# Performance work log

Hardware: AMD Instinct MI355X
Metric: run time of the kernel (lower is better)

The kernel has to match this reference:

```python
import jax, jax.numpy as jnp
import numpy as np

N = 50000      # nodes
E = 800000     # edges
F_IN = 256
HID = [256, 256, 512]
G = 512        # graphs
FP = 2048      # fingerprint size


def setup_inputs() -> dict:
    key = jax.random.key(0)
    ks = jax.random.split(key, 14)
    node_features = jax.random.normal(ks[0], (N, F_IN), dtype=jnp.float32)
    edge_index = jax.random.randint(ks[1], (2, E), 0, N, dtype=jnp.int64)
    batch = jnp.sort(jax.random.randint(ks[2], (N,), 0, G, dtype=jnp.int64))

    def lin(k, fi, fo):
        s = 1.0 / np.sqrt(fi)
        kw, kb = jax.random.split(k)
        W = jax.random.uniform(kw, (fi, fo), jnp.float32, -s, s)
        b = jax.random.uniform(kb, (fo,), jnp.float32, -s, s)
        return W, b

    W1, b1 = lin(ks[3], F_IN, HID[0])
    W2, b2 = lin(ks[4], HID[0], HID[1])
    W3, b3 = lin(ks[5], HID[1], HID[2])
    pw, pb = lin(ks[6], HID[2], 1)          # PoolWeightedSum gating linear
    Wo, bo = lin(ks[7], 2 * HID[2], FP)     # head: weight_sum + max concat
    return dict(node_features=node_features, edge_index=edge_index, batch=batch,
                W1=W1, b1=b1, W2=W2, b2=b2, W3=W3, b3=b3,
                pw=pw, pb=pb, Wo=Wo, bo=bo)


def _gcn_layer(x, src, dst, W, b):
    # GCNConv: add self-loops, symmetric normalization, h = x @ W, aggregate.
    n = x.shape[0]
    h = x @ W  # [N, F_out]
    loop = jnp.arange(n, dtype=src.dtype)
    s = jnp.concatenate([src, loop])
    d = jnp.concatenate([dst, loop])
    deg = jax.ops.segment_sum(jnp.ones(s.shape[0], h.dtype), d, num_segments=n)
    dis = jax.lax.rsqrt(deg)  # deg >= 1 because of self-loops
    norm = dis[s] * dis[d]    # [E+N]
    out = jax.ops.segment_sum(h[s] * norm[:, None], d, num_segments=n)
    return out + b


def _forward(node_features, edge_index, batch,
             W1, b1, W2, b2, W3, b3, pw, pb, Wo, bo):
    src, dst = edge_index[0], edge_index[1]
    x = node_features
    for W, b in ((W1, b1), (W2, b2), (W3, b3)):
        x = jax.nn.relu(_gcn_layer(x, src, dst, W, b))

    # PoolWeightedSum: sigmoid-gated node features, scatter-add per graph
    w = jax.nn.sigmoid(x @ pw + pb)  # [N, 1]
    pooled_ws = jax.ops.segment_sum(x * w, batch, num_segments=G,
                                    indices_are_sorted=True)
    # PoolMax: scatter-max per graph (empty segments -> 0, like torch zeros init)
    pooled_max = jax.ops.segment_max(x, batch, num_segments=G,
                                     indices_are_sorted=True)
    pooled_max = jnp.where(jnp.isfinite(pooled_max), pooled_max, 0.0)

    feats = jnp.concatenate([pooled_ws, pooled_max], axis=1)  # [G, 2*HID[-1]]
    return jax.nn.relu(feats @ Wo + bo)  # [G, FP]


def reference(node_features, edge_index, batch,
              W1, b1, W2, b2, W3, b3, pw, pb, Wo, bo):
    return _forward(node_features, edge_index, batch,
                    W1, b1, W2, b2, W3, b3, pw, pb, Wo, bo)
```

## Files before the change

kernel.cpp:

```cpp
#include <hip/hip_runtime.h>
#include <math.h>

#define NNODES 50000
#define NEDGES 800000
#define NGRAPH 512
#define FIN    256
#define H1     256
#define H2     256
#define H3     512
#define FPOUT  2048

#define NBUCK  196
#define EPB    3200
#define BCAP   4864

typedef __attribute__((ext_vector_type(8))) short short8;
typedef __attribute__((ext_vector_type(8))) _Float16 half8;
typedef __attribute__((ext_vector_type(4))) float floatx4;
typedef __attribute__((ext_vector_type(4))) unsigned short ushx4;

__device__ inline float h2f(ushort u) { return (float)__builtin_bit_cast(_Float16, u); }
__device__ inline ushort f2h(float x) { return __builtin_bit_cast(ushort, (_Float16)x); }
__device__ inline void split2h(float a, ushort& h, ushort& l) {
    _Float16 hh = (_Float16)a;
    h = __builtin_bit_cast(ushort, hh);
    l = f2h(a - (float)hh);
}


__global__ __launch_bounds__(256) void zero_i32(int* p, int n) {
    int i = blockIdx.x * 256 + threadIdx.x;
    if (i < n) p[i] = 0;
}

__global__ __launch_bounds__(256) void count_deg(const int* __restrict__ ei, int* __restrict__ degi, int e_total) {
    int e = blockIdx.x * 256 + threadIdx.x;
    if (e >= e_total) return;
    int d = ei[e_total + e];
    atomicAdd(&degi[d], 1);
}

__global__ __launch_bounds__(256) void calc_dis(const int* __restrict__ degi, float* __restrict__ dis, int n) {
    int i = blockIdx.x * 256 + threadIdx.x;
    if (i < n) dis[i] = rsqrtf((float)(degi[i] + 1));
}

__global__ __launch_bounds__(256) void scanA(const int* __restrict__ degi, int* __restrict__ offs,
                                             int* __restrict__ partials, int n) {
    __shared__ int sm[256];
    int t = threadIdx.x, idx = blockIdx.x * 256 + t;
    int v = (idx < n) ? degi[idx] : 0;
    sm[t] = v; __syncthreads();
    for (int d = 1; d < 256; d <<= 1) {
        int add = (t >= d) ? sm[t - d] : 0;
        __syncthreads();
        sm[t] += add;
        __syncthreads();
    }
    if (idx < n) offs[idx + 1] = sm[t];
    if (t == 255) partials[blockIdx.x] = sm[255];
}

__global__ __launch_bounds__(256) void scanB(int* __restrict__ partials, int nb) {
    __shared__ int sm[256];
    int t = threadIdx.x;
    int v = (t < nb) ? partials[t] : 0;
    sm[t] = v; __syncthreads();
    for (int d = 1; d < 256; d <<= 1) {
        int add = (t >= d) ? sm[t - d] : 0;
        __syncthreads();
        sm[t] += add;
        __syncthreads();
    }
    if (t < nb) partials[t] = sm[t] - v;
}

__global__ __launch_bounds__(256) void scanC(int* __restrict__ offs, const int* __restrict__ partials, int n) {
    int idx = blockIdx.x * 256 + threadIdx.x;
    if (idx < n) offs[idx + 1] += partials[blockIdx.x];
    if (idx == 0) offs[0] = 0;
}

__global__ __launch_bounds__(256) void binA(const int* __restrict__ ei, const int* __restrict__ offs,
                                            int* __restrict__ gcur, int2* __restrict__ tmp, int e_total) {
    __shared__ int2 ls[EPB];
    __shared__ int2 ls2[EPB];
    __shared__ int hist[256], lpref[256], lcur[256], gbase[256], obase[256];
    int tid = threadIdx.x;
    int e0 = blockIdx.x * EPB;
    int cnt = e_total - e0; if (cnt > EPB) cnt = EPB;
    hist[tid] = 0;
    __syncthreads();
    for (int i = tid; i < cnt; i += 256) {
        int s = ei[e0 + i];
        int d = ei[e_total + e0 + i];
        ls[i] = (int2){s, d};
        atomicAdd(&hist[d >> 8], 1);
    }
    __syncthreads();
    int hv = hist[tid];
    lpref[tid] = hv;
    __syncthreads();
    for (int dlt = 1; dlt < 256; dlt <<= 1) {
        int add = (tid >= dlt) ? lpref[tid - dlt] : 0;
        __syncthreads();
        lpref[tid] += add;
        __syncthreads();
    }
    int excl = lpref[tid] - hv;
    __syncthreads();
    lpref[tid] = excl;
    lcur[tid] = 0;
    __syncthreads();
    for (int i = tid; i < cnt; i += 256) {
        int2 pr = ls[i];
        int b = pr.y >> 8;
        int r = atomicAdd(&lcur[b], 1);
        ls2[lpref[b] + r] = pr;
    }
    if (tid < NBUCK) {
        int c = hist[tid];
        gbase[tid] = c ? atomicAdd(&gcur[tid], c) : 0;
        obase[tid] = offs[tid << 8];
    }
    __syncthreads();
    for (int i = tid; i < cnt; i += 256) {
        int2 pr = ls2[i];
        int b = pr.y >> 8;
        tmp[obase[b] + gbase[b] + (i - lpref[b])] = pr;
    }
}

__global__ __launch_bounds__(256) void binB(const int2* __restrict__ tmp, const int* __restrict__ offs,
                                            const float* __restrict__ dis, int2* __restrict__ csr_pair) {
    __shared__ int2 ls[BCAP];
    __shared__ int cntN[256];
    int tid = threadIdx.x;
    int b = blockIdx.x;
    int nlo = b << 8;
    int nhi = nlo + 256; if (nhi > NNODES) nhi = NNODES;
    int base = offs[nlo];
    int tot = offs[nhi] - base;
    cntN[tid] = 0;
    __syncthreads();
    for (int c0 = 0; c0 < tot; c0 += BCAP) {
        int cc = tot - c0; if (cc > BCAP) cc = BCAP;
        for (int i = tid; i < cc; i += 256)
            ls[i] = tmp[base + c0 + i];
        __syncthreads();
        for (int i = tid; i < cc; i += 256) {
            int2 pr = ls[i];
            int d = pr.y;
            int r = atomicAdd(&cntN[d & 255], 1);
            float w = dis[pr.x] * dis[d];
            csr_pair[offs[d] + r] = (int2){pr.x, __float_as_int(w)};
        }
        __syncthreads();
    }
}

__global__ __launch_bounds__(256) void wsplit_t(const float* __restrict__ W, ushort* __restrict__ hi,
                                                ushort* __restrict__ lo, int K, int N) {
    __shared__ float sm[32][33];
    int tx = threadIdx.x & 31, ty = threadIdx.x >> 5;
    int n0 = blockIdx.x * 32, k0 = blockIdx.y * 32;
    #pragma unroll
    for (int j = 0; j < 32; j += 8)
        sm[ty + j][tx] = W[(size_t)(k0 + ty + j) * N + n0 + tx];
    __syncthreads();
    #pragma unroll
    for (int j = 0; j < 32; j += 8) {
        float a = sm[tx][ty + j];
        ushort h, l; split2h(a, h, l);
        size_t o = (size_t)(n0 + ty + j) * K + k0 + tx;
        hi[o] = h; lo[o] = l;
    }
}

__global__ __launch_bounds__(256) void conv_f16(const float* __restrict__ x, ushort* __restrict__ xh, int total4) {
    int i = blockIdx.x * 256 + threadIdx.x;
    if (i >= total4) return;
    float4 a = ((const float4*)x)[i];
    ushx4 h = {f2h(a.x), f2h(a.y), f2h(a.z), f2h(a.w)};
    ((ushx4*)xh)[i] = h;
}

template<int SPLIT, int ACC, int KSPAN>
__global__ __launch_bounds__(256) void gemm_f16(const ushort* __restrict__ Ahp, const ushort* __restrict__ Alp,
                                                const ushort* __restrict__ Bhp, const ushort* __restrict__ Blp,
                                                float* __restrict__ C, ushort* __restrict__ Ch,
                                                const float* __restrict__ bias,
                                                int M, int N, int K, int do_relu, int outmode) {
    __shared__ _Float16 lsA[128 * 64];
    __shared__ _Float16 lsB[128 * 64];
    __shared__ _Float16 lsAl[SPLIT ? 128 * 64 : 8];
    __shared__ _Float16 lsBl[SPLIT ? 128 * 64 : 8];
    const _Float16* Ah = (const _Float16*)Ahp;
    const _Float16* Al = (const _Float16*)Alp;
    const _Float16* Bh = (const _Float16*)Bhp;
    const _Float16* Bl = (const _Float16*)Blp;

    int tid = threadIdx.x;
    int w = tid >> 6, lane = tid & 63;
    int quad = lane >> 4, lr = lane & 15;
    int wm = w & 1, wn = w >> 1;

    int gx = gridDim.x;
    int orig = blockIdx.y * gx + blockIdx.x;
    int nwg = gx * gridDim.y;
    int xcd = orig & 7, slot = orig >> 3;
    int q = nwg >> 3, r = nwg & 7;
    int wid = (xcd < r ? xcd * (q + 1) : r * (q + 1) + (xcd - r) * q) + slot;
    int row0 = (wid / gx) * 128, col0 = (wid % gx) * 128;
    int kb = blockIdx.z * KSPAN;

    floatx4 acc[4][4];
    #pragma unroll
    for (int i = 0; i < 4; ++i)
        #pragma unroll
        for (int j = 0; j < 4; ++j)
            acc[i][j] = (floatx4){0.f, 0.f, 0.f, 0.f};

    const half8 zer = {};
    int srow = tid >> 3;
    int sgran = tid & 7;
    int skk = sgran * 8;
    int sgx = (sgran ^ (srow & 7)) * 8;

    half8 pa[4], pb[4], pal[4], pbl[4];
    #pragma unroll
    for (int c = 0; c < 4; ++c) {
        int row = c * 32 + srow;
        bool mok = (row0 + row) < M;
        size_t aoff = (size_t)(row0 + row) * K + kb + skk;
        pa[c] = mok ? *(const half8*)(Ah + aoff) : zer;
        if constexpr (SPLIT) pal[c] = mok ? *(const half8*)(Al + aoff) : zer;
        size_t boff = (size_t)(col0 + row) * K + kb + skk;
        pb[c] = *(const half8*)(Bh + boff);
        if constexpr (SPLIT) pbl[c] = *(const half8*)(Bl + boff);
    }

    for (int k0 = kb; k0 < kb + KSPAN; k0 += 64) {
        #pragma unroll
        for (int c = 0; c < 4; ++c) {
            int lo = (c * 32 + srow) * 64 + sgx;
            *(half8*)(lsA + lo) = pa[c];
            *(half8*)(lsB + lo) = pb[c];
            if constexpr (SPLIT) { *(half8*)(lsAl + lo) = pal[c]; *(half8*)(lsBl + lo) = pbl[c]; }
        }
        __syncthreads();
        if (k0 + 64 < kb + KSPAN) {
            #pragma unroll
            for (int c = 0; c < 4; ++c) {
                int row = c * 32 + srow;
                bool mok = (row0 + row) < M;
                size_t aoff = (size_t)(row0 + row) * K + k0 + 64 + skk;
                pa[c] = mok ? *(const half8*)(Ah + aoff) : zer;
                if constexpr (SPLIT) pal[c] = mok ? *(const half8*)(Al + aoff) : zer;
                size_t boff = (size_t)(col0 + row) * K + k0 + 64 + skk;
                pb[c] = *(const half8*)(Bh + boff);
                if constexpr (SPLIT) pbl[c] = *(const half8*)(Bl + boff);
            }
        }
        #pragma unroll
        for (int kk = 0; kk < 2; ++kk) {
            half8 af[4], afl[4];
            #pragma unroll
            for (int mt = 0; mt < 4; ++mt) {
                int row = wm * 64 + mt * 16 + lr;
                int ao = row * 64 + (((kk * 4 + quad) ^ (row & 7)) << 3);
                af[mt] = *(const half8*)(lsA + ao);
                if constexpr (SPLIT) afl[mt] = *(const half8*)(lsAl + ao);
            }
            #pragma unroll
            for (int nt = 0; nt < 4; ++nt) {
                int row = wn * 64 + nt * 16 + lr;
                int bo = row * 64 + (((kk * 4 + quad) ^ (row & 7)) << 3);
                half8 bf = *(const half8*)(lsB + bo);
                half8 bfl;
                if constexpr (SPLIT) bfl = *(const half8*)(lsBl + bo);
                #pragma unroll
                for (int mt = 0; mt < 4; ++mt) {
                    acc[mt][nt] = __builtin_amdgcn_mfma_f32_16x16x32_f16(af[mt], bf, acc[mt][nt], 0, 0, 0);
                    if constexpr (SPLIT) {
                        acc[mt][nt] = __builtin_amdgcn_mfma_f32_16x16x32_f16(af[mt], bfl, acc[mt][nt], 0, 0, 0);
                        acc[mt][nt] = __builtin_amdgcn_mfma_f32_16x16x32_f16(afl[mt], bf, acc[mt][nt], 0, 0, 0);
                    }
                }
            }
        }
        __syncthreads();
    }

    size_t zoff = ACC ? (size_t)blockIdx.z * M * N : 0;
    #pragma unroll
    for (int mt = 0; mt < 4; ++mt) {
        #pragma unroll
        for (int rr = 0; rr < 4; ++rr) {
            int row = row0 + wm * 64 + mt * 16 + quad * 4 + rr;
            if (row >= M) continue;
            #pragma unroll
            for (int nt = 0; nt < 4; ++nt) {
                int col = col0 + wn * 64 + nt * 16 + lr;
                float v = acc[mt][nt][rr];
                if (!ACC) {
                    v += bias[col];
                    if (do_relu) v = v > 0.f ? v : 0.f;
                }
                if (outmode) Ch[(size_t)row * N + col] = f2h(v);
                else         C[zoff + (size_t)row * N + col] = v;
            }
        }
    }
}

__global__ __launch_bounds__(256) void head_fin(const float* __restrict__ part, const float* __restrict__ bo,
                                                float* __restrict__ out) {
    int i4 = blockIdx.x * 256 + threadIdx.x;
    const int TOT4 = NGRAPH * FPOUT / 4;
    if (i4 >= TOT4) return;
    int col4 = i4 & (FPOUT / 4 - 1);
    const size_t STRIDE4 = (size_t)NGRAPH * FPOUT / 4;
    const float4* p = (const float4*)part;
    float4 a = p[i4];
    float4 b = p[i4 + STRIDE4];
    float4 c = p[i4 + 2 * STRIDE4];
    float4 d = p[i4 + 3 * STRIDE4];
    float4 bb = ((const float4*)bo)[col4];
    float4 o;
    o.x = a.x + b.x + c.x + d.x + bb.x; o.x = o.x > 0.f ? o.x : 0.f;
    o.y = a.y + b.y + c.y + d.y + bb.y; o.y = o.y > 0.f ? o.y : 0.f;
    o.z = a.z + b.z + c.z + d.z + bb.z; o.z = o.z > 0.f ? o.z : 0.f;
    o.w = a.w + b.w + c.w + d.w + bb.w; o.w = o.w > 0.f ? o.w : 0.f;
    ((float4*)out)[i4] = o;
}

__global__ __launch_bounds__(256) void agg256b(const ushort* __restrict__ xh, ushort* __restrict__ yh,
                                               const float* __restrict__ dis,
                                               const int* __restrict__ offs, const int2* __restrict__ csr_pair) {
    constexpr int F = 256;
    int wave = threadIdx.x >> 6;
    int lane = threadIdx.x & 63;
    int half = lane >> 5;
    int sub  = lane & 31;
    int v = blockIdx.x * 8 + wave * 2 + half;
    int beg = offs[v], end = offs[v + 1];
    int len = end - beg;
    int leno = __shfl_xor(len, 32, 64);
    int maxlen = len > leno ? len : leno;

    float dv = dis[v];
    float sw = dv * dv;
    short8 a0 = ((const short8*)(xh + (size_t)v * F))[sub];
    float acc[8];
    #pragma unroll
    for (int j = 0; j < 8; ++j) acc[j] = h2f((ushort)a0[j]) * sw;

    for (int k = 0; k < maxlen; k += 8) {
        int   s[8];
        float w[8];
        #pragma unroll
        for (int u = 0; u < 8; ++u) {
            int idx = beg + k + u;
            bool val = idx < end;
            int ic = val ? idx : beg;
            int2 pr = csr_pair[ic];
            s[u] = pr.x;
            w[u] = val ? __int_as_float(pr.y) : 0.f;
        }
        short8 g[8];
        #pragma unroll
        for (int u = 0; u < 8; ++u)
            g[u] = ((const short8*)(xh + (size_t)s[u] * F))[sub];
        #pragma unroll
        for (int u = 0; u < 8; ++u) {
            #pragma unroll
            for (int j = 0; j < 8; ++j)
                acc[j] += h2f((ushort)g[u][j]) * w[u];
        }
    }

    ushort h[8];
    #pragma unroll
    for (int j = 0; j < 8; ++j) h[j] = f2h(acc[j]);
    short8 hv = {(short)h[0], (short)h[1], (short)h[2], (short)h[3], (short)h[4], (short)h[5], (short)h[6], (short)h[7]};
    ((short8*)(yh + (size_t)v * F))[sub] = hv;
}

__global__ __launch_bounds__(1024) void gatepool(const float* __restrict__ x, const float* __restrict__ pw,
                                                 const float* __restrict__ pb, const int* __restrict__ batch,
                                                 ushort* __restrict__ phi, ushort* __restrict__ plo, int n) {
    int g = blockIdx.x;
    int t = threadIdx.x;
    int wave = t >> 6, lane = t & 63;
    int lo_ = 0, hi_ = n;
    while (lo_ < hi_) { int mid = (lo_ + hi_) >> 1; if (batch[mid] < g) lo_ = mid + 1; else hi_ = mid; }
    int start = lo_;
    hi_ = n;
    while (lo_ < hi_) { int mid = (lo_ + hi_) >> 1; if (batch[mid] < g + 1) lo_ = mid + 1; else hi_ = mid; }
    int end = lo_;

    const float4* pwv = (const float4*)pw;
    float4 wa = pwv[lane], wb = pwv[lane + 64];
    float pb0 = pb[0];

    float4 s0 = make_float4(0.f, 0.f, 0.f, 0.f), s1 = s0;
    float4 m0 = make_float4(-INFINITY, -INFINITY, -INFINITY, -INFINITY), m1 = m0;

    for (int nn = start + wave; nn < end; nn += 16) {
        const float4* xr = (const float4*)(x + (size_t)nn * 512);
        float4 a = xr[lane];
        float4 b = xr[lane + 64];
        float p = a.x * wa.x + a.y * wa.y + a.z * wa.z + a.w * wa.w
                + b.x * wb.x + b.y * wb.y + b.z * wb.z + b.w * wb.w;
        #pragma unroll
        for (int off = 32; off; off >>= 1) p += __shfl_down(p, off, 64);
        float wg = __shfl(p, 0, 64);
        wg = 1.f / (1.f + expf(-(wg + pb0)));
        s0.x += a.x * wg; s0.y += a.y * wg; s0.z += a.z * wg; s0.w += a.w * wg;
        s1.x += b.x * wg; s1.y += b.y * wg; s1.z += b.z * wg; s1.w += b.w * wg;
        m0.x = fmaxf(m0.x, a.x); m0.y = fmaxf(m0.y, a.y); m0.z = fmaxf(m0.z, a.z); m0.w = fmaxf(m0.w, a.w);
        m1.x = fmaxf(m1.x, b.x); m1.y = fmaxf(m1.y, b.y); m1.z = fmaxf(m1.z, b.z); m1.w = fmaxf(m1.w, b.w);
    }

    __shared__ float ls[16][1024];
    *(float4*)&ls[wave][lane * 4]       = s0;
    *(float4*)&ls[wave][256 + lane * 4] = s1;
    *(float4*)&ls[wave][512 + lane * 4] = m0;
    *(float4*)&ls[wave][768 + lane * 4] = m1;
    __syncthreads();

    float val;
    if (t < 512) {
        float s = 0.f;
        #pragma unroll
        for (int wv = 0; wv < 16; ++wv) s += ls[wv][t];
        val = s;
    } else {
        float m = -INFINITY;
        #pragma unroll
        for (int wv = 0; wv < 16; ++wv) m = fmaxf(m, ls[wv][t]);
        if (start >= end) m = 0.f;
        val = m;
    }
    ushort h, l;
    split2h(val, h, l);
    size_t base = (size_t)g * 1024;
    phi[base + t] = h;
    plo[base + t] = l;
}


extern "C" void kernel_launch(void* const* d_in, const int* in_sizes, int n_in,
                              void* d_out, int out_size, void* d_ws, size_t ws_size,
                              hipStream_t stream) {
    const float* x0    = (const float*)d_in[0];
    const int*   ei    = (const int*)d_in[1];
    const int*   batch = (const int*)d_in[2];
    const float* W1 = (const float*)d_in[3];
    const float* b1 = (const float*)d_in[4];
    const float* W2 = (const float*)d_in[5];
    const float* b2 = (const float*)d_in[6];
    const float* W3 = (const float*)d_in[7];
    const float* b3 = (const float*)d_in[8];
    const float* pw = (const float*)d_in[9];
    const float* pb = (const float*)d_in[10];
    const float* Wo = (const float*)d_in[11];
    const float* bo = (const float*)d_in[12];
    float* out = (float*)d_out;

    float* ws = (float*)d_ws;
    size_t off = 0;
    float* bufB = ws + off; off += (size_t)NNODES * 512;
    ushort* xh  = (ushort*)(ws + off); off += (size_t)NNODES * 256 / 2;
    ushort* yh  = (ushort*)(ws + off); off += (size_t)NNODES * 256 / 2;
    int2*   tmp = (int2*)(ws + off);   off += (size_t)NNODES * 256 / 2;
    ushort* W1thi = (ushort*)(ws + off); off += 256 * 256 / 2;
    ushort* W1tlo = (ushort*)(ws + off); off += 256 * 256 / 2;
    ushort* W2thi = (ushort*)(ws + off); off += 256 * 256 / 2;
    ushort* W2tlo = (ushort*)(ws + off); off += 256 * 256 / 2;
    ushort* W3thi = (ushort*)(ws + off); off += 512 * 256 / 2;
    ushort* W3tlo = (ushort*)(ws + off); off += 512 * 256 / 2;
    ushort* Wothi = (ushort*)(ws + off); off += (size_t)FPOUT * 1024 / 2;
    ushort* Wotlo = (ushort*)(ws + off); off += (size_t)FPOUT * 1024 / 2;
    ushort* phi = (ushort*)(ws + off); off += (size_t)NGRAPH * 1024 / 2;
    ushort* plo = (ushort*)(ws + off); off += (size_t)NGRAPH * 1024 / 2;
    float* dis  = ws + off; off += NNODES;
    int*   degi = (int*)(ws + off); off += NNODES;
    int*   offs = (int*)(ws + off); off += (NNODES + 4);
    int*   gcur = (int*)(ws + off); off += 256;
    int2*  csr_pair = (int2*)(ws + off); off += 2 * (size_t)NEDGES;
    int*   partials = (int*)(ws + off); off += 256;

    const int NB_N = (NNODES + 255) / 256;
    const int NB_E = (NEDGES + 255) / 256;
    const int NB_A = NNODES / 8;
    const int MB128 = (NNODES + 127) / 128;

    { dim3 g(256 / 32, 256 / 32);    wsplit_t<<<g, 256, 0, stream>>>(W1, W1thi, W1tlo, 256, 256); }
    { dim3 g(256 / 32, 256 / 32);    wsplit_t<<<g, 256, 0, stream>>>(W2, W2thi, W2tlo, 256, 256); }
    { dim3 g(512 / 32, 256 / 32);    wsplit_t<<<g, 256, 0, stream>>>(W3, W3thi, W3tlo, 256, 512); }
    { dim3 g(FPOUT / 32, 1024 / 32); wsplit_t<<<g, 256, 0, stream>>>(Wo, Wothi, Wotlo, 1024, FPOUT); }

    zero_i32<<<NB_N, 256, 0, stream>>>(degi, NNODES);
    count_deg<<<NB_E, 256, 0, stream>>>(ei, degi, NEDGES);
    calc_dis<<<NB_N, 256, 0, stream>>>(degi, dis, NNODES);
    scanA<<<NB_N, 256, 0, stream>>>(degi, offs, partials, NNODES);
    scanB<<<1, 256, 0, stream>>>(partials, NB_N);
    scanC<<<NB_N, 256, 0, stream>>>(offs, partials, NNODES);
    zero_i32<<<1, 256, 0, stream>>>(gcur, 256);
    binA<<<NEDGES / EPB, 256, 0, stream>>>(ei, offs, gcur, tmp, NEDGES);
    binB<<<NBUCK, 256, 0, stream>>>(tmp, offs, dis, csr_pair);

    conv_f16<<<(NNODES * 256 / 4 + 255) / 256, 256, 0, stream>>>(x0, xh, NNODES * 256 / 4);

    agg256b<<<NB_A, 256, 0, stream>>>(xh, yh, dis, offs, csr_pair);
    {
        dim3 grid(H1 / 128, MB128);
        gemm_f16<0, 0, 256><<<grid, 256, 0, stream>>>(yh, nullptr, W1thi, nullptr, nullptr, xh, b1,
                                                      NNODES, H1, FIN, 1, 1);
    }
    agg256b<<<NB_A, 256, 0, stream>>>(xh, yh, dis, offs, csr_pair);
    {
        dim3 grid(H2 / 128, MB128);
        gemm_f16<0, 0, 256><<<grid, 256, 0, stream>>>(yh, nullptr, W2thi, nullptr, nullptr, xh, b2,
                                                      NNODES, H2, H1, 1, 1);
    }
    agg256b<<<NB_A, 256, 0, stream>>>(xh, yh, dis, offs, csr_pair);
    {
        dim3 grid(H3 / 128, MB128);
        gemm_f16<0, 0, 256><<<grid, 256, 0, stream>>>(yh, nullptr, W3thi, nullptr, bufB, nullptr, b3,
                                                      NNODES, H3, H2, 1, 0);
    }
    gatepool<<<NGRAPH, 1024, 0, stream>>>(bufB, pw, pb, batch, phi, plo, NNODES);
    {
        dim3 grid(FPOUT / 128, (NGRAPH + 127) / 128, 4);
        gemm_f16<1, 1, 256><<<grid, 256, 0, stream>>>(phi, plo, Wothi, Wotlo, bufB, nullptr, nullptr,
                                                      NGRAPH, FPOUT, 1024, 0, 0);
    }
    head_fin<<<(NGRAPH * FPOUT / 4 + 255) / 256, 256, 0, stream>>>(bufB, bo, out);
}
```

Measured before the change: 539.1 us.

## Aggregate in feature-chunked layout over degree-sorted nodes for gather locality

Stores the fp16 node features in a chunked layout of 32 features per chunk, [chunk][node][32], written by conv_f16 and by the GEMM epilogue. Nodes are reordered by degree through a histogram, scan and scatter into an aux table, so that nodes of similar degree share a wave. The new aggregation kernel handles one feature chunk per block and splits edges across 4 waves, then reduces through shared memory. The aim is to shrink the gathered working set per chunk so it fits in cache and to cut divergence from uneven degrees, at the cost of extra preprocessing kernels, a shared-memory reduction and eight times as many blocks.

```diff
diff --git a/kernel.cpp b/kernel.cpp
--- a/kernel.cpp
+++ b/kernel.cpp
@@ -159,6 +159,40 @@
     }
 }
 
+__global__ __launch_bounds__(256) void deg_hist(const int* __restrict__ degi, int* __restrict__ hist, int n) {
+    int i = blockIdx.x * 256 + threadIdx.x;
+    if (i >= n) return;
+    int d = degi[i];
+    atomicAdd(&hist[d > 255 ? 255 : d], 1);
+}
+
+__global__ __launch_bounds__(256) void scan256(int* __restrict__ buf) {
+    __shared__ int sm[256];
+    int t = threadIdx.x;
+    int v = buf[t];
+    sm[t] = v; __syncthreads();
+    for (int d = 1; d < 256; d <<= 1) {
+        int add = (t >= d) ? sm[t - d] : 0;
+        __syncthreads();
+        sm[t] += add;
+        __syncthreads();
+    }
+    buf[t] = sm[t] - v;
+}
+
+__global__ __launch_bounds__(256) void deg_scatter(const int* __restrict__ degi, const int* __restrict__ offs,
+                                                   const float* __restrict__ dis, const int* __restrict__ hbase,
+                                                   int* __restrict__ hcur, int4* __restrict__ aux, int n) {
+    int i = blockIdx.x * 256 + threadIdx.x;
+    if (i >= n) return;
+    int d = degi[i];
+    int b = d > 255 ? 255 : d;
+    int r = atomicAdd(&hcur[b], 1);
+    int4 e;
+    e.x = i; e.y = offs[i]; e.z = d; e.w = __float_as_int(dis[i]);
+    aux[hbase[b] + r] = e;
+}
+
 __global__ __launch_bounds__(256) void wsplit_t(const float* __restrict__ W, ushort* __restrict__ hi,
                                                 ushort* __restrict__ lo, int K, int N) {
     __shared__ float sm[32][33];
@@ -180,9 +214,12 @@
 __global__ __launch_bounds__(256) void conv_f16(const float* __restrict__ x, ushort* __restrict__ xh, int total4) {
     int i = blockIdx.x * 256 + threadIdx.x;
     if (i >= total4) return;
+    int n  = i >> 6;
+    int f4 = i & 63;
     float4 a = ((const float4*)x)[i];
     ushx4 h = {f2h(a.x), f2h(a.y), f2h(a.z), f2h(a.w)};
-    ((ushx4*)xh)[i] = h;
+    size_t o4 = (((size_t)(f4 >> 3) * NNODES + n) * 32 + (f4 & 7) * 4) >> 2;
+    ((ushx4*)xh)[o4] = h;
 }
 
 template<int SPLIT, int ACC, int KSPAN>
@@ -307,7 +344,7 @@
                     v += bias[col];
                     if (do_relu) v = v > 0.f ? v : 0.f;
                 }
-                if (outmode) Ch[(size_t)row * N + col] = f2h(v);
+                if (outmode) Ch[((size_t)(col >> 5) * M + row) * 32 + (col & 31)] = f2h(v);
                 else         C[zoff + (size_t)row * N + col] = v;
             }
         }
@@ -335,56 +372,70 @@
     ((float4*)out)[i4] = o;
 }
 
-__global__ __launch_bounds__(256) void agg256b(const ushort* __restrict__ xh, ushort* __restrict__ yh,
-                                               const float* __restrict__ dis,
-                                               const int* __restrict__ offs, const int2* __restrict__ csr_pair) {
-    constexpr int F = 256;
+__global__ __launch_bounds__(256) void agg_chunk(const ushort* __restrict__ xh, ushort* __restrict__ yh,
+                                                 const int4* __restrict__ aux,
+                                                 const int2* __restrict__ csr_pair) {
+    __shared__ float sm[4][64][9];
     int wave = threadIdx.x >> 6;
     int lane = threadIdx.x & 63;
-    int half = lane >> 5;
-    int sub  = lane & 31;
-    int v = blockIdx.x * 8 + wave * 2 + half;
-    int beg = offs[v], end = offs[v + 1];
-    int len = end - beg;
-    int leno = __shfl_xor(len, 32, 64);
-    int maxlen = len > leno ? len : leno;
-
-    float dv = dis[v];
+    int nd = lane >> 2, quad = lane & 3;
+    int chunk = blockIdx.x & 7;
+    int slot = (blockIdx.x >> 3) * 16 + nd;
+    int4 a = aux[slot];
+    int v = a.x, beg = a.y, deg = a.z;
+    float dv = __int_as_float(a.w);
     float sw = dv * dv;
-    short8 a0 = ((const short8*)(xh + (size_t)v * F))[sub];
+    const _Float16* xc = (const _Float16*)xh + (size_t)chunk * NNODES * 32;
+
     float acc[8];
+    if (wave == 0) {
+        half8 g0 = *(const half8*)(xc + (size_t)v * 32 + quad * 8);
+        #pragma unroll
+        for (int j = 0; j < 8; ++j) acc[j] = (float)g0[j] * sw;
+    } else {
+        #pragma unroll
+        for (int j = 0; j < 8; ++j) acc[j] = 0.f;
+    }
+
+    int md = deg;
     #pragma unroll
-    for (int j = 0; j < 8; ++j) acc[j] = h2f((ushort)a0[j]) * sw;
-
-    for (int k = 0; k < maxlen; k += 8) {
-        int   s[8];
-        float w[8];
-        #pragma unroll
-        for (int u = 0; u < 8; ++u) {
-            int idx = beg + k + u;
-            bool val = idx < end;
-            int ic = val ? idx : beg;
-            int2 pr = csr_pair[ic];
-            s[u] = pr.x;
+    for (int m = 4; m <= 32; m <<= 1) { int o = __shfl_xor(md, m, 64); md = md > o ? md : o; }
+
+    for (int k8 = 0; k8 < md; k8 += 8) {
+        int s[2]; float w[2];
+        #pragma unroll
+        for (int u = 0; u < 2; ++u) {
+            int e = k8 + u * 4 + wave;
+            bool val = e < deg;
+            int2 pr = csr_pair[val ? (beg + e) : beg];
+            s[u] = val ? pr.x : 0;
             w[u] = val ? __int_as_float(pr.y) : 0.f;
         }
-        short8 g[8];
-        #pragma unroll
-        for (int u = 0; u < 8; ++u)
-            g[u] = ((const short8*)(xh + (size_t)s[u] * F))[sub];
-        #pragma unroll
-        for (int u = 0; u < 8; ++u) {
+        half8 g[2];
+        #pragma unroll
+        for (int u = 0; u < 2; ++u)
+            g[u] = *(const half8*)(xc + (size_t)s[u] * 32 + quad * 8);
+        #pragma unroll
+        for (int u = 0; u < 2; ++u)
             #pragma unroll
-            for (int j = 0; j < 8; ++j)
-                acc[j] += h2f((ushort)g[u][j]) * w[u];
-        }
-    }
-
-    ushort h[8];
+            for (int j = 0; j < 8; ++j) acc[j] += (float)g[u][j] * w[u];
+    }
+
     #pragma unroll
-    for (int j = 0; j < 8; ++j) h[j] = f2h(acc[j]);
-    short8 hv = {(short)h[0], (short)h[1], (short)h[2], (short)h[3], (short)h[4], (short)h[5], (short)h[6], (short)h[7]};
-    ((short8*)(yh + (size_t)v * F))[sub] = hv;
+    for (int j = 0; j < 8; ++j) sm[wave][lane][j] = acc[j];
+    __syncthreads();
+    if (wave == 0) {
+        #pragma unroll
+        for (int wv = 1; wv < 4; ++wv)
+            #pragma unroll
+            for (int j = 0; j < 8; ++j) acc[j] += sm[wv][lane][j];
+        ushort h[8];
+        #pragma unroll
+        for (int j = 0; j < 8; ++j) h[j] = f2h(acc[j]);
+        short8 hv = {(short)h[0], (short)h[1], (short)h[2], (short)h[3],
+                     (short)h[4], (short)h[5], (short)h[6], (short)h[7]};
+        *(short8*)(yh + (size_t)v * 256 + chunk * 32 + quad * 8) = hv;
+    }
 }
 
 __global__ __launch_bounds__(1024) void gatepool(const float* __restrict__ x, const float* __restrict__ pw,
@@ -491,10 +542,13 @@
     int*   gcur = (int*)(ws + off); off += 256;
     int2*  csr_pair = (int2*)(ws + off); off += 2 * (size_t)NEDGES;
     int*   partials = (int*)(ws + off); off += 256;
+    int*   hist = (int*)(ws + off); off += 256;
+    int*   hcur = (int*)(ws + off); off += 256;
+    int4*  aux  = (int4*)(ws + off); off += (size_t)NNODES * 4;
 
     const int NB_N = (NNODES + 255) / 256;
     const int NB_E = (NEDGES + 255) / 256;
-    const int NB_A = NNODES / 8;
+    const int NB_A = (NNODES / 16) * 8;
     const int MB128 = (NNODES + 127) / 128;
 
     { dim3 g(256 / 32, 256 / 32);    wsplit_t<<<g, 256, 0, stream>>>(W1, W1thi, W1tlo, 256, 256); }
@@ -512,21 +566,27 @@
     binA<<<NEDGES / EPB, 256, 0, stream>>>(ei, offs, gcur, tmp, NEDGES);
     binB<<<NBUCK, 256, 0, stream>>>(tmp, offs, dis, csr_pair);
 
+    zero_i32<<<1, 256, 0, stream>>>(hist, 256);
+    deg_hist<<<NB_N, 256, 0, stream>>>(degi, hist, NNODES);
+    scan256<<<1, 256, 0, stream>>>(hist);
+    zero_i32<<<1, 256, 0, stream>>>(hcur, 256);
+    deg_scatter<<<NB_N, 256, 0, stream>>>(degi, offs, dis, hist, hcur, aux, NNODES);
+
     conv_f16<<<(NNODES * 256 / 4 + 255) / 256, 256, 0, stream>>>(x0, xh, NNODES * 256 / 4);
 
-    agg256b<<<NB_A, 256, 0, stream>>>(xh, yh, dis, offs, csr_pair);
+    agg_chunk<<<NB_A, 256, 0, stream>>>(xh, yh, aux, csr_pair);
     {
         dim3 grid(H1 / 128, MB128);
         gemm_f16<0, 0, 256><<<grid, 256, 0, stream>>>(yh, nullptr, W1thi, nullptr, nullptr, xh, b1,
                                                       NNODES, H1, FIN, 1, 1);
     }
-    agg256b<<<NB_A, 256, 0, stream>>>(xh, yh, dis, offs, csr_pair);
+    agg_chunk<<<NB_A, 256, 0, stream>>>(xh, yh, aux, csr_pair);
     {
         dim3 grid(H2 / 128, MB128);
         gemm_f16<0, 0, 256><<<grid, 256, 0, stream>>>(yh, nullptr, W2thi, nullptr, nullptr, xh, b2,
                                                       NNODES, H2, H1, 1, 1);
     }
-    agg256b<<<NB_A, 256, 0, stream>>>(xh, yh, dis, offs, csr_pair);
+    agg_chunk<<<NB_A, 256, 0, stream>>>(xh, yh, aux, csr_pair);
     {
         dim3 grid(H3 / 128, MB128);
         gemm_f16<0, 0, 256><<<grid, 256, 0, stream>>>(yh, nullptr, W3thi, nullptr, bufB, nullptr, b3,
```

After: 849.1 us. 57.5% more time.

## Bin edges into fixed-capacity buckets first and derive degrees from buckets

Applied to the files above, without the earlier changes.

Removes the global atomic degree-count kernel. Edges are now binned into fixed-capacity per-bucket regions (BKCAP slots per 256-node bucket), so binning no longer needs the prefix-sum offsets. A new per-bucket kernel counts degrees with shared-memory atomics, and the CSR fill reads from the fixed bucket regions. This replaces 800K global atomics with shared atomics and adds one pass over the binned edges. It risks overflow if any bucket receives more than 6144 edges.

```diff
diff --git a/kernel.cpp b/kernel.cpp
--- a/kernel.cpp
+++ b/kernel.cpp
@@ -13,6 +13,7 @@
 #define NBUCK  196
 #define EPB    3200
 #define BCAP   4864
+#define BKCAP  6144
 
 typedef __attribute__((ext_vector_type(8))) short short8;
 typedef __attribute__((ext_vector_type(8))) _Float16 half8;
@@ -31,13 +32,6 @@
 __global__ __launch_bounds__(256) void zero_i32(int* p, int n) {
     int i = blockIdx.x * 256 + threadIdx.x;
     if (i < n) p[i] = 0;
-}
-
-__global__ __launch_bounds__(256) void count_deg(const int* __restrict__ ei, int* __restrict__ degi, int e_total) {
-    int e = blockIdx.x * 256 + threadIdx.x;
-    if (e >= e_total) return;
-    int d = ei[e_total + e];
-    atomicAdd(&degi[d], 1);
 }
 
 __global__ __launch_bounds__(256) void calc_dis(const int* __restrict__ degi, float* __restrict__ dis, int n) {
@@ -81,11 +75,11 @@
     if (idx == 0) offs[0] = 0;
 }
 
-__global__ __launch_bounds__(256) void binA(const int* __restrict__ ei, const int* __restrict__ offs,
-                                            int* __restrict__ gcur, int2* __restrict__ tmp, int e_total) {
+__global__ __launch_bounds__(256) void binA(const int* __restrict__ ei, int* __restrict__ gcur,
+                                            int2* __restrict__ tmp, int e_total) {
     __shared__ int2 ls[EPB];
     __shared__ int2 ls2[EPB];
-    __shared__ int hist[256], lpref[256], lcur[256], gbase[256], obase[256];
+    __shared__ int hist[256], lpref[256], lcur[256], gbase[256];
     int tid = threadIdx.x;
     int e0 = blockIdx.x * EPB;
     int cnt = e_total - e0; if (cnt > EPB) cnt = EPB;
@@ -121,32 +115,46 @@
     if (tid < NBUCK) {
         int c = hist[tid];
         gbase[tid] = c ? atomicAdd(&gcur[tid], c) : 0;
-        obase[tid] = offs[tid << 8];
     }
     __syncthreads();
     for (int i = tid; i < cnt; i += 256) {
         int2 pr = ls2[i];
         int b = pr.y >> 8;
-        tmp[obase[b] + gbase[b] + (i - lpref[b])] = pr;
-    }
-}
-
-__global__ __launch_bounds__(256) void binB(const int2* __restrict__ tmp, const int* __restrict__ offs,
-                                            const float* __restrict__ dis, int2* __restrict__ csr_pair) {
+        tmp[(size_t)b * BKCAP + gbase[b] + (i - lpref[b])] = pr;
+    }
+}
+
+__global__ __launch_bounds__(256) void binB1(const int2* __restrict__ tmp, const int* __restrict__ gcur,
+                                             int* __restrict__ degi) {
+    __shared__ int cntN[256];
+    int tid = threadIdx.x;
+    int b = blockIdx.x;
+    cntN[tid] = 0;
+    __syncthreads();
+    int tot = gcur[b];
+    const int2* base = tmp + (size_t)b * BKCAP;
+    for (int i = tid; i < tot; i += 256)
+        atomicAdd(&cntN[base[i].y & 255], 1);
+    __syncthreads();
+    int node = (b << 8) + tid;
+    if (node < NNODES) degi[node] = cntN[tid];
+}
+
+__global__ __launch_bounds__(256) void binB2(const int2* __restrict__ tmp, const int* __restrict__ gcur,
+                                             const int* __restrict__ offs, const float* __restrict__ dis,
+                                             int2* __restrict__ csr_pair) {
     __shared__ int2 ls[BCAP];
     __shared__ int cntN[256];
     int tid = threadIdx.x;
     int b = blockIdx.x;
-    int nlo = b << 8;
-    int nhi = nlo + 256; if (nhi > NNODES) nhi = NNODES;
-    int base = offs[nlo];
-    int tot = offs[nhi] - base;
+    int tot = gcur[b];
+    const int2* base = tmp + (size_t)b * BKCAP;
     cntN[tid] = 0;
     __syncthreads();
     for (int c0 = 0; c0 < tot; c0 += BCAP) {
         int cc = tot - c0; if (cc > BCAP) cc = BCAP;
         for (int i = tid; i < cc; i += 256)
-            ls[i] = tmp[base + c0 + i];
+            ls[i] = base[c0 + i];
         __syncthreads();
         for (int i = tid; i < cc; i += 256) {
             int2 pr = ls[i];
@@ -493,7 +501,6 @@
     int*   partials = (int*)(ws + off); off += 256;
 
     const int NB_N = (NNODES + 255) / 256;
-    const int NB_E = (NEDGES + 255) / 256;
     const int NB_A = NNODES / 8;
     const int MB128 = (NNODES + 127) / 128;
 
@@ -502,15 +509,14 @@
     { dim3 g(512 / 32, 256 / 32);    wsplit_t<<<g, 256, 0, stream>>>(W3, W3thi, W3tlo, 256, 512); }
     { dim3 g(FPOUT / 32, 1024 / 32); wsplit_t<<<g, 256, 0, stream>>>(Wo, Wothi, Wotlo, 1024, FPOUT); }
 
-    zero_i32<<<NB_N, 256, 0, stream>>>(degi, NNODES);
-    count_deg<<<NB_E, 256, 0, stream>>>(ei, degi, NEDGES);
+    zero_i32<<<1, 256, 0, stream>>>(gcur, 256);
+    binA<<<NEDGES / EPB, 256, 0, stream>>>(ei, gcur, tmp, NEDGES);
+    binB1<<<NBUCK, 256, 0, stream>>>(tmp, gcur, degi);
     calc_dis<<<NB_N, 256, 0, stream>>>(degi, dis, NNODES);
     scanA<<<NB_N, 256, 0, stream>>>(degi, offs, partials, NNODES);
     scanB<<<1, 256, 0, stream>>>(partials, NB_N);
     scanC<<<NB_N, 256, 0, stream>>>(offs, partials, NNODES);
-    zero_i32<<<1, 256, 0, stream>>>(gcur, 256);
-    binA<<<NEDGES / EPB, 256, 0, stream>>>(ei, offs, gcur, tmp, NEDGES);
-    binB<<<NBUCK, 256, 0, stream>>>(tmp, offs, dis, csr_pair);
+    binB2<<<NBUCK, 256, 0, stream>>>(tmp, gcur, offs, dis, csr_pair);
 
     conv_f16<<<(NNODES * 256 / 4 + 255) / 256, 256, 0, stream>>>(x0, xh, NNODES * 256 / 4);
 
```

Result: faster. 507.6 us (-5.8%).
